# Kernel optimization log

Hardware: AMD Instinct MI355X
Metric: run time of the kernel (lower is better)

The kernel has to match this reference:

```python
import jax, jax.numpy as jnp
import numpy as np

N_NODES = 50000
N_EDGES = 600000
N_GRAPHS = 1000
IN_DIM = 16
HID = 128
DESC = 17
NUM_LAYERS = 3
BN_EPS = 1e-5


def setup_inputs() -> dict:
    key = jax.random.key(0)
    ks = jax.random.split(key, 16)
    x = jax.random.normal(ks[0], (N_NODES, IN_DIM), dtype=jnp.float32)
    edge_index = jax.random.randint(ks[1], (2, N_EDGES), 0, N_NODES, dtype=jnp.int32)
    edge_attr = jax.random.normal(ks[2], (N_EDGES, HID), dtype=jnp.float32)
    batch = jnp.sort(jax.random.randint(ks[3], (N_NODES,), 0, N_GRAPHS, dtype=jnp.int32))
    mol_desc = jax.random.normal(ks[4], (N_GRAPHS, DESC), dtype=jnp.float32)
    s = 1.0 / np.sqrt(HID)
    Wp = jax.random.normal(ks[5], (IN_DIM, HID), dtype=jnp.float32) / np.sqrt(IN_DIM)
    bp = jnp.zeros((HID,), jnp.float32)
    W1 = jax.random.normal(ks[6], (NUM_LAYERS, HID, HID), dtype=jnp.float32) * s
    b1 = jnp.zeros((NUM_LAYERS, HID), jnp.float32)
    W2 = jax.random.normal(ks[7], (NUM_LAYERS, HID, HID), dtype=jnp.float32) * s
    b2 = jnp.zeros((NUM_LAYERS, HID), jnp.float32)
    gamma = jnp.ones((NUM_LAYERS, HID), jnp.float32)
    beta = jnp.zeros((NUM_LAYERS, HID), jnp.float32)
    Wf = jax.random.normal(ks[8], (HID + DESC, 1), dtype=jnp.float32) / np.sqrt(HID + DESC)
    bf = jnp.zeros((1,), jnp.float32)
    return dict(x=x, edge_index=edge_index, edge_attr=edge_attr, batch=batch,
                mol_desc=mol_desc, Wp=Wp, bp=bp, W1=W1, b1=b1, W2=W2, b2=b2,
                gamma=gamma, beta=beta, Wf=Wf, bf=bf)


def reference(x, edge_index, edge_attr, batch, mol_desc,
              Wp, bp, W1, b1, W2, b2, gamma, beta, Wf, bf):
    src, dst = edge_index[0], edge_index[1]
    h = x @ Wp + bp  # [N, HID]
    for l in range(NUM_LAYERS):
        # GINEConv: aggr_i = sum_j relu(h_j + e_ij); out = MLP((1+eps)*h + aggr), eps=0
        msg = jax.nn.relu(h[src] + edge_attr)                       # [E, HID] gather
        aggr = jax.ops.segment_sum(msg, dst, num_segments=N_NODES)  # scatter-add
        z = h + aggr
        z = jax.nn.relu(z @ W1[l] + b1[l]) @ W2[l] + b2[l]
        # BatchNorm1d (training-mode batch statistics)
        mean = jnp.mean(z, axis=0)
        var = jnp.var(z, axis=0)
        z = (z - mean) * jax.lax.rsqrt(var + BN_EPS) * gamma[l] + beta[l]
        h = jax.nn.relu(z)  # dropout = identity (eval)
    # global mean pool per graph
    sums = jax.ops.segment_sum(h, batch, num_segments=N_GRAPHS)
    counts = jax.ops.segment_sum(jnp.ones((N_NODES,), h.dtype), batch, num_segments=N_GRAPHS)
    pooled = sums / jnp.maximum(counts, 1.0)[:, None]
    feats = jnp.concatenate([pooled, mol_desc], axis=1)  # [G, HID+DESC]
    return (feats @ Wf + bf).squeeze(-1)  # [G]
```

## Files before the change

kernel.cpp:

```cpp
#include <hip/hip_runtime.h>
#include <hip/hip_bf16.h>

#define NN 50000
#define NE 600000
#define NG 1000
#define IND 16
#define HID 128
#define DESCD 17
#define NL 3
#define BN_EPS 1e-5f
#define NB_SCAN 196

typedef short s16x8 __attribute__((ext_vector_type(8)));
typedef float f32x4 __attribute__((ext_vector_type(4)));
typedef float f32x2 __attribute__((ext_vector_type(2)));
typedef __hip_bfloat16 bfp16;
typedef __hip_bfloat162 bfp162;

__global__ __launch_bounds__(256) void k_hist(const int* __restrict__ dst,
                                              int* __restrict__ deg) {
    int e = blockIdx.x * blockDim.x + threadIdx.x;
    if (e >= NE) return;
    atomicAdd(&deg[dst[e]], 1);
}

__global__ __launch_bounds__(256) void k_part(const int* __restrict__ deg,
                                              int* __restrict__ partials) {
    __shared__ int sh[256];
    int i = blockIdx.x * 256 + threadIdx.x;
    sh[threadIdx.x] = (i < NN) ? deg[i] : 0;
    __syncthreads();
    for (int o = 128; o > 0; o >>= 1) {
        if (threadIdx.x < o) sh[threadIdx.x] += sh[threadIdx.x + o];
        __syncthreads();
    }
    if (threadIdx.x == 0) partials[blockIdx.x] = sh[0];
}

__global__ __launch_bounds__(256) void k_scanpart(const int* __restrict__ partials,
                                                  int* __restrict__ poffs) {
    __shared__ int sh[256];
    int t = threadIdx.x;
    int v = (t < NB_SCAN) ? partials[t] : 0;
    sh[t] = v;
    __syncthreads();
    for (int o = 1; o < 256; o <<= 1) {
        int tmp = (t >= o) ? sh[t - o] : 0;
        __syncthreads();
        sh[t] += tmp;
        __syncthreads();
    }
    if (t < NB_SCAN) poffs[t] = sh[t] - v;
}

__global__ __launch_bounds__(256) void k_scatter(const int* __restrict__ deg,
                                                 const int* __restrict__ poffs,
                                                 int* __restrict__ rowptr,
                                                 int* __restrict__ cursor) {
    __shared__ int sh[256];
    int b = blockIdx.x, t = threadIdx.x;
    int i = b * 256 + t;
    int v = (i < NN) ? deg[i] : 0;
    sh[t] = v;
    __syncthreads();
    for (int o = 1; o < 256; o <<= 1) {
        int tmp = (t >= o) ? sh[t - o] : 0;
        __syncthreads();
        sh[t] += tmp;
        __syncthreads();
    }
    int excl = sh[t] - v + poffs[b];
    if (i < NN) {
        rowptr[i] = excl;
        cursor[i] = excl;
        if (i == NN - 1) rowptr[NN] = excl + v;
    }
}

__global__ __launch_bounds__(256) void k_fill(const int* __restrict__ src,
                                              const int* __restrict__ dst,
                                              int* __restrict__ cursor,
                                              int2* __restrict__ perm) {
    int e = blockIdx.x * blockDim.x + threadIdx.x;
    if (e >= NE) return;
    int pos = atomicAdd(&cursor[dst[e]], 1);
    perm[pos] = make_int2(e, src[e]);
}

__global__ __launch_bounds__(256) void k_wprep(const float* __restrict__ W1,
                                               const float* __restrict__ W2,
                                               bfp16* __restrict__ Wt) {
    int id = blockIdx.x * blockDim.x + threadIdx.x;
    if (id >= 6 * HID * HID) return;
    int m = id >> 14;
    int rem = id & 16383;
    int n = rem >> 7, k = rem & 127;
    const float* Wsrc = (m < 3) ? (W1 + (size_t)m * HID * HID)
                                : (W2 + (size_t)(m - 3) * HID * HID);
    Wt[id] = __float2bfloat16(Wsrc[k * HID + n]);
}

__global__ __launch_bounds__(256) void k_proj(const float* __restrict__ x,
                                              const float* __restrict__ Wp,
                                              const float* __restrict__ bp,
                                              bfp16* __restrict__ h) {
    int idx = blockIdx.x * blockDim.x + threadIdx.x;
    if (idx >= NN * HID) return;
    int row = idx >> 7, col = idx & 127;
    const float* xr = x + (size_t)row * IND;
    float acc = bp[col];
#pragma unroll
    for (int k = 0; k < IND; k++) acc += xr[k] * Wp[k * HID + col];
    h[idx] = __float2bfloat16(acc);
}

template <int MODE, bool BN>
__global__ __launch_bounds__(256) void k_aggr(const bfp16* __restrict__ hz,
                                              const float* __restrict__ ea,
                                              bfp162* __restrict__ eab2,
                                              const int2* __restrict__ perm,
                                              const int* __restrict__ rowptr,
                                              const float* __restrict__ stats,
                                              const float* __restrict__ gamma,
                                              const float* __restrict__ beta,
                                              bfp16* __restrict__ z) {
    int nid = (blockIdx.x * blockDim.x + threadIdx.x) >> 6;
    int lane = threadIdx.x & 63;
    if (nid >= NN) return;
    const int f = lane * 2;

    float sc0 = 0.f, sf0 = 0.f, sc1 = 0.f, sf1 = 0.f;
    if (BN) {
        const float invn = 1.f / NN;
        float m0 = stats[f] * invn;
        float v0 = stats[128 + f] * invn - m0 * m0;
        sc0 = rsqrtf(v0 + BN_EPS) * gamma[f];
        sf0 = beta[f] - m0 * sc0;
        float m1 = stats[f + 1] * invn;
        float v1 = stats[128 + f + 1] * invn - m1 * m1;
        sc1 = rsqrtf(v1 + BN_EPS) * gamma[f + 1];
        sf1 = beta[f + 1] - m1 * sc1;
    }

    int beg = rowptr[nid], end = rowptr[nid + 1];
    float ax = 0.f, ay = 0.f;
    int i = beg;
    for (; i + 3 < end; i += 4) {
#pragma unroll
        for (int u = 0; u < 4; u++) {
            int2 pr = perm[i + u];
            float2 a;
            if (MODE == 2) {
                a = __bfloat1622float2(eab2[(size_t)(i + u) * 64 + lane]);
            } else {
                f32x2 av = __builtin_nontemporal_load(
                        (const f32x2*)&ea[(size_t)pr.x * HID + f]);
                a = make_float2(av.x, av.y);
                eab2[(size_t)(i + u) * 64 + lane] = __float22bfloat162_rn(a);
            }
            float2 hv = __bfloat1622float2(*(const bfp162*)&hz[(size_t)pr.y * HID + f]);
            if (BN) {
                hv.x = fmaxf(hv.x * sc0 + sf0, 0.f);
                hv.y = fmaxf(hv.y * sc1 + sf1, 0.f);
            }
            ax += fmaxf(a.x + hv.x, 0.f);
            ay += fmaxf(a.y + hv.y, 0.f);
        }
    }
    for (; i < end; i++) {
        int2 pr = perm[i];
        float2 a;
        if (MODE == 2) {
            a = __bfloat1622float2(eab2[(size_t)i * 64 + lane]);
        } else {
            f32x2 av = __builtin_nontemporal_load(
                    (const f32x2*)&ea[(size_t)pr.x * HID + f]);
            a = make_float2(av.x, av.y);
            eab2[(size_t)i * 64 + lane] = __float22bfloat162_rn(a);
        }
        float2 hv = __bfloat1622float2(*(const bfp162*)&hz[(size_t)pr.y * HID + f]);
        if (BN) {
            hv.x = fmaxf(hv.x * sc0 + sf0, 0.f);
            hv.y = fmaxf(hv.y * sc1 + sf1, 0.f);
        }
        ax += fmaxf(a.x + hv.x, 0.f);
        ay += fmaxf(a.y + hv.y, 0.f);
    }
    float2 hn = __bfloat1622float2(*(const bfp162*)&hz[(size_t)nid * HID + f]);
    if (BN) {
        hn.x = fmaxf(hn.x * sc0 + sf0, 0.f);
        hn.y = fmaxf(hn.y * sc1 + sf1, 0.f);
    }
    *(bfp162*)&z[(size_t)nid * HID + f] =
        __float22bfloat162_rn(make_float2(ax + hn.x, ay + hn.y));
}

__global__ __launch_bounds__(256) void k_mlp(const bfp16* __restrict__ A,
                                             const bfp16* __restrict__ Wt1,
                                             const bfp16* __restrict__ Wt2,
                                             const float* __restrict__ b1,
                                             const float* __restrict__ b2,
                                             bfp16* __restrict__ z2,
                                             float* __restrict__ stats,
                                             int N) {
    __shared__ __align__(16) short sW1[128 * 128];
    __shared__ __align__(16) short sW2[128 * 128];
    __shared__ __align__(16) short sA[64 * 128];
    const int t = threadIdx.x;
    const int rowBase = blockIdx.x * 64;

    const short* W1g = (const short*)Wt1;
    const short* W2g = (const short*)Wt2;
    for (int g = t; g < 2048; g += 256) {
        int nrow = g >> 4, s = g & 15;
        int sw = nrow * 128 + ((s ^ (nrow & 7)) << 3);
        *(float4*)&sW1[sw] = *(const float4*)&W1g[g * 8];
        *(float4*)&sW2[sw] = *(const float4*)&W2g[g * 8];
    }
    const short* Ag = (const short*)A;
    for (int g = t; g < 1024; g += 256) {
        int r = g >> 4, s = g & 15;
        float4 v = make_float4(0.f, 0.f, 0.f, 0.f);
        if (rowBase + r < N) v = *(const float4*)&Ag[(size_t)(rowBase + r) * 128 + s * 8];
        *(float4*)&sA[r * 128 + ((s ^ (r & 7)) << 3)] = v;
    }
    __syncthreads();

    const int w = t >> 6, lane = t & 63;
    const int l15 = lane & 15, lhi = lane >> 4;
    const int arow = (w << 4) + l15;
    const int abase = arow * 128, asw = arow & 7;
    const int bsw = l15 & 7;

    f32x4 acc[8];
#pragma unroll
    for (int c = 0; c < 8; c++) acc[c] = (f32x4){0.f, 0.f, 0.f, 0.f};
#pragma unroll
    for (int kk = 0; kk < 4; kk++) {
        int kslot = kk * 4 + lhi;
        s16x8 af = *(const s16x8*)&sA[abase + ((kslot ^ asw) << 3)];
#pragma unroll
        for (int c = 0; c < 8; c++) {
            s16x8 bfr = *(const s16x8*)&sW1[(c * 16 + l15) * 128 + ((kslot ^ bsw) << 3)];
            acc[c] = __builtin_amdgcn_mfma_f32_16x16x32_bf16(af, bfr, acc[c], 0, 0, 0);
        }
    }
    __syncthreads();

    {
        const int rowb = (w << 4);
#pragma unroll
        for (int c = 0; c < 8; c++) {
            float bb = b1[c * 16 + l15];
            int col = c * 16 + l15;
#pragma unroll
            for (int r = 0; r < 4; r++) {
                int row = rowb + lhi * 4 + r;
                float v = fmaxf(acc[c][r] + bb, 0.f);
                bfp16 bv = __float2bfloat16(v);
                sA[row * 128 + ((((col >> 3)) ^ (row & 7)) << 3) + (col & 7)] =
                    *reinterpret_cast<short*>(&bv);
            }
        }
    }
    __syncthreads();

    f32x4 acc2[8];
#pragma unroll
    for (int c = 0; c < 8; c++) acc2[c] = (f32x4){0.f, 0.f, 0.f, 0.f};
#pragma unroll
    for (int kk = 0; kk < 4; kk++) {
        int kslot = kk * 4 + lhi;
        s16x8 af = *(const s16x8*)&sA[abase + ((kslot ^ asw) << 3)];
#pragma unroll
        for (int c = 0; c < 8; c++) {
            s16x8 bfr = *(const s16x8*)&sW2[(c * 16 + l15) * 128 + ((kslot ^ bsw) << 3)];
            acc2[c] = __builtin_amdgcn_mfma_f32_16x16x32_bf16(af, bfr, acc2[c], 0, 0, 0);
        }
    }

    const int rb = rowBase + (w << 4) + lhi * 4;
    float scol[8], qcol[8];
#pragma unroll
    for (int c = 0; c < 8; c++) {
        float bb = b2[c * 16 + l15];
        float s = 0.f, q = 0.f;
#pragma unroll
        for (int r = 0; r < 4; r++) {
            int row = rb + r;
            float v = acc2[c][r] + bb;
            if (row < N) {
                z2[(size_t)row * 128 + c * 16 + l15] = __float2bfloat16(v);
                s += v;
                q += v * v;
            }
        }
        scol[c] = s;
        qcol[c] = q;
    }
#pragma unroll
    for (int c = 0; c < 8; c++) {
        scol[c] += __shfl_xor(scol[c], 16);
        scol[c] += __shfl_xor(scol[c], 32);
        qcol[c] += __shfl_xor(qcol[c], 16);
        qcol[c] += __shfl_xor(qcol[c], 32);
    }
    __syncthreads();
    float* sStat = (float*)sA;
    if (lane < 16) {
#pragma unroll
        for (int c = 0; c < 8; c++) {
            sStat[w * 256 + c * 16 + lane] = scol[c];
            sStat[w * 256 + 128 + c * 16 + lane] = qcol[c];
        }
    }
    __syncthreads();
    if (t < 128) {
        float ss = sStat[t] + sStat[256 + t] + sStat[512 + t] + sStat[768 + t];
        float qq = sStat[128 + t] + sStat[384 + t] + sStat[640 + t] + sStat[896 + t];
        atomicAdd(&stats[t], ss);
        atomicAdd(&stats[128 + t], qq);
    }
}

__global__ __launch_bounds__(256) void k_finalpool(const bfp16* __restrict__ z2,
                                                   const float* __restrict__ stats,
                                                   const float* __restrict__ gamma,
                                                   const float* __restrict__ beta,
                                                   const int* __restrict__ batch,
                                                   const float* __restrict__ mol,
                                                   const float* __restrict__ Wf,
                                                   const float* __restrict__ bfp,
                                                   float* __restrict__ out) {
    int gid = (blockIdx.x * blockDim.x + threadIdx.x) >> 6;
    int lane = threadIdx.x & 63;
    if (gid >= NG) return;
    const int f = lane * 2;

    const float invn = 1.f / NN;
    float m0 = stats[f] * invn;
    float v0 = stats[128 + f] * invn - m0 * m0;
    float sc0 = rsqrtf(v0 + BN_EPS) * gamma[f];
    float sf0 = beta[f] - m0 * sc0;
    float m1 = stats[f + 1] * invn;
    float v1 = stats[128 + f + 1] * invn - m1 * m1;
    float sc1 = rsqrtf(v1 + BN_EPS) * gamma[f + 1];
    float sf1 = beta[f + 1] - m1 * sc1;

    int lo = 0, hi = NN;
    while (lo < hi) { int m = (lo + hi) >> 1; if (batch[m] < gid) lo = m + 1; else hi = m; }
    int lb = lo;
    hi = NN;
    while (lo < hi) { int m = (lo + hi) >> 1; if (batch[m] <= gid) lo = m + 1; else hi = m; }
    int cnt = lo - lb;

    float sx = 0.f, sy = 0.f;
    for (int n = lb; n < lo; n++) {
        float2 v = __bfloat1622float2(*(const bfp162*)&z2[(size_t)n * HID + f]);
        sx += fmaxf(v.x * sc0 + sf0, 0.f);
        sy += fmaxf(v.y * sc1 + sf1, 0.f);
    }
    float inv = 1.f / fmaxf((float)cnt, 1.f);
    float acc = sx * inv * Wf[f] + sy * inv * Wf[f + 1];
    if (lane < DESCD) acc += mol[(size_t)gid * DESCD + lane] * Wf[HID + lane];
#pragma unroll
    for (int o = 32; o > 0; o >>= 1) acc += __shfl_down(acc, o);
    if (lane == 0) out[gid] = acc + bfp[0];
}

extern "C" void kernel_launch(void* const* d_in, const int* in_sizes, int n_in,
                              void* d_out, int out_size, void* d_ws, size_t ws_size,
                              hipStream_t stream) {
    const float* x     = (const float*)d_in[0];
    const int*   ei    = (const int*)d_in[1];
    const float* ea    = (const float*)d_in[2];
    const int*   batch = (const int*)d_in[3];
    const float* mol   = (const float*)d_in[4];
    const float* Wp    = (const float*)d_in[5];
    const float* bp    = (const float*)d_in[6];
    const float* W1    = (const float*)d_in[7];
    const float* b1    = (const float*)d_in[8];
    const float* W2    = (const float*)d_in[9];
    const float* b2    = (const float*)d_in[10];
    const float* gamma = (const float*)d_in[11];
    const float* beta  = (const float*)d_in[12];
    const float* Wf    = (const float*)d_in[13];
    const float* bf_   = (const float*)d_in[14];
    float* out = (float*)d_out;

    char* p = (char*)d_ws;
    size_t off = 0;
    auto alloc = [&](size_t bytes) {
        char* q = p + off;
        off = (off + bytes + 255) & ~(size_t)255;
        return q;
    };
    bfp16* h      = (bfp16*)alloc((size_t)NN * HID * 2);
    bfp16* z      = (bfp16*)alloc((size_t)NN * HID * 2);
    bfp16* z2     = (bfp16*)alloc((size_t)NN * HID * 2);
    bfp16* Wt     = (bfp16*)alloc((size_t)6 * HID * HID * 2);
    int2*  perm   = (int2*)alloc((size_t)NE * 8);
    int*   rowptr = (int*)alloc((NN + 16) * 4);
    int*   cursor = (int*)alloc(NN * 4);
    int*   partials = (int*)alloc(NB_SCAN * 4);
    int*   poffs    = (int*)alloc(NB_SCAN * 4);
    size_t zoff = off;
    int*   deg    = (int*)alloc(NN * 4);
    float* stats3 = (float*)alloc(3 * 256 * 4);
    size_t zlen = off - zoff;
    bfp162* eab2 = (bfp162*)alloc((size_t)NE * HID * 2);

    const int* src = ei;
    const int* dst = ei + NE;

    (void)hipMemsetAsync(p + zoff, 0, zlen, stream);
    k_hist<<<(NE + 255) / 256, 256, 0, stream>>>(dst, deg);
    k_part<<<NB_SCAN, 256, 0, stream>>>(deg, partials);
    k_scanpart<<<1, 256, 0, stream>>>(partials, poffs);
    k_scatter<<<NB_SCAN, 256, 0, stream>>>(deg, poffs, rowptr, cursor);
    k_fill<<<(NE + 255) / 256, 256, 0, stream>>>(src, dst, cursor, perm);
    k_wprep<<<(6 * HID * HID + 255) / 256, 256, 0, stream>>>(W1, W2, Wt);
    k_proj<<<(NN * HID) / 256, 256, 0, stream>>>(x, Wp, bp, h);

    const int aggrGrid = (NN * 64) / 256;
    const int mlpGrid = (NN + 63) / 64;
    for (int l = 0; l < NL; l++) {
        if (l == 0)
            k_aggr<1, false><<<aggrGrid, 256, 0, stream>>>(
                h, ea, eab2, perm, rowptr, nullptr, nullptr, nullptr, z);
        else
            k_aggr<2, true><<<aggrGrid, 256, 0, stream>>>(
                z2, nullptr, eab2, perm, rowptr, stats3 + (l - 1) * 256,
                gamma + (l - 1) * HID, beta + (l - 1) * HID, z);
        k_mlp<<<mlpGrid, 256, 0, stream>>>(
            z, Wt + (size_t)l * HID * HID, Wt + (size_t)(3 + l) * HID * HID,
            b1 + l * HID, b2 + l * HID, z2, stats3 + l * 256, NN);
    }

    k_finalpool<<<(NG * 64) / 256, 256, 0, stream>>>(
        z2, stats3 + 2 * 256, gamma + 2 * HID, beta + 2 * HID,
        batch, mol, Wf, bf_, out);
}
```

Measured before the change: 431.8 us.

## Split wavefront into four edge slots with 16-byte vector loads in aggregation

The aggregation kernel now gives each 16-lane group its own edge, with every lane handling 8 features through 16-byte loads of edge attributes and neighbour rows. The four partial sums are combined with cross-lane shuffles, and only 16 lanes write the output row. The aim is more memory-level parallelism per wavefront and fewer, wider memory transactions on the gather-heavy loop. Separately, the projection and weight-prep kernels are merged into a single launch to save one kernel launch. The cost is 16 extra accumulator and BN registers per lane, extra shuffles, and idle lanes for nodes with few edges.

After: 431.6 us. About the same (-0.1%).

```diff
diff --git a/kernel.cpp b/kernel.cpp
--- a/kernel.cpp
+++ b/kernel.cpp
@@ -13,9 +13,13 @@
 
 typedef short s16x8 __attribute__((ext_vector_type(8)));
 typedef float f32x4 __attribute__((ext_vector_type(4)));
-typedef float f32x2 __attribute__((ext_vector_type(2)));
+typedef int   i32x4 __attribute__((ext_vector_type(4)));
 typedef __hip_bfloat16 bfp16;
 typedef __hip_bfloat162 bfp162;
+
+__device__ __forceinline__ float b2f(short s) {
+    return __uint_as_float(((unsigned int)(unsigned short)s) << 16);
+}
 
 __global__ __launch_bounds__(256) void k_hist(const int* __restrict__ dst,
                                               int* __restrict__ deg) {
@@ -87,37 +91,39 @@
     perm[pos] = make_int2(e, src[e]);
 }
 
-__global__ __launch_bounds__(256) void k_wprep(const float* __restrict__ W1,
-                                               const float* __restrict__ W2,
-                                               bfp16* __restrict__ Wt) {
-    int id = blockIdx.x * blockDim.x + threadIdx.x;
-    if (id >= 6 * HID * HID) return;
-    int m = id >> 14;
-    int rem = id & 16383;
-    int n = rem >> 7, k = rem & 127;
-    const float* Wsrc = (m < 3) ? (W1 + (size_t)m * HID * HID)
-                                : (W2 + (size_t)(m - 3) * HID * HID);
-    Wt[id] = __float2bfloat16(Wsrc[k * HID + n]);
-}
-
-__global__ __launch_bounds__(256) void k_proj(const float* __restrict__ x,
-                                              const float* __restrict__ Wp,
-                                              const float* __restrict__ bp,
-                                              bfp16* __restrict__ h) {
-    int idx = blockIdx.x * blockDim.x + threadIdx.x;
-    if (idx >= NN * HID) return;
-    int row = idx >> 7, col = idx & 127;
-    const float* xr = x + (size_t)row * IND;
-    float acc = bp[col];
-#pragma unroll
-    for (int k = 0; k < IND; k++) acc += xr[k] * Wp[k * HID + col];
-    h[idx] = __float2bfloat16(acc);
+__global__ __launch_bounds__(256) void k_projwprep(const float* __restrict__ x,
+                                                   const float* __restrict__ Wp,
+                                                   const float* __restrict__ bp,
+                                                   bfp16* __restrict__ h,
+                                                   const float* __restrict__ W1,
+                                                   const float* __restrict__ W2,
+                                                   bfp16* __restrict__ Wt,
+                                                   int projBlocks) {
+    if (blockIdx.x < (unsigned)projBlocks) {
+        int idx = blockIdx.x * blockDim.x + threadIdx.x;
+        if (idx >= NN * HID) return;
+        int row = idx >> 7, col = idx & 127;
+        const float* xr = x + (size_t)row * IND;
+        float acc = bp[col];
+#pragma unroll
+        for (int k = 0; k < IND; k++) acc += xr[k] * Wp[k * HID + col];
+        h[idx] = __float2bfloat16(acc);
+    } else {
+        int id = (blockIdx.x - projBlocks) * blockDim.x + threadIdx.x;
+        if (id >= 6 * HID * HID) return;
+        int m = id >> 14;
+        int rem = id & 16383;
+        int n = rem >> 7, k = rem & 127;
+        const float* Wsrc = (m < 3) ? (W1 + (size_t)m * HID * HID)
+                                    : (W2 + (size_t)(m - 3) * HID * HID);
+        Wt[id] = __float2bfloat16(Wsrc[k * HID + n]);
+    }
 }
 
 template <int MODE, bool BN>
 __global__ __launch_bounds__(256) void k_aggr(const bfp16* __restrict__ hz,
                                               const float* __restrict__ ea,
-                                              bfp162* __restrict__ eab2,
+                                              bfp16* __restrict__ eab,
                                               const int2* __restrict__ perm,
                                               const int* __restrict__ rowptr,
                                               const float* __restrict__ stats,
@@ -127,72 +133,95 @@
     int nid = (blockIdx.x * blockDim.x + threadIdx.x) >> 6;
     int lane = threadIdx.x & 63;
     if (nid >= NN) return;
-    const int f = lane * 2;
-
-    float sc0 = 0.f, sf0 = 0.f, sc1 = 0.f, sf1 = 0.f;
+    const int slot = lane >> 4;
+    const int c0 = (lane & 15) << 3;
+
+    float sc[8], sf[8];
     if (BN) {
         const float invn = 1.f / NN;
-        float m0 = stats[f] * invn;
-        float v0 = stats[128 + f] * invn - m0 * m0;
-        sc0 = rsqrtf(v0 + BN_EPS) * gamma[f];
-        sf0 = beta[f] - m0 * sc0;
-        float m1 = stats[f + 1] * invn;
-        float v1 = stats[128 + f + 1] * invn - m1 * m1;
-        sc1 = rsqrtf(v1 + BN_EPS) * gamma[f + 1];
-        sf1 = beta[f + 1] - m1 * sc1;
-    }
+#pragma unroll
+        for (int j = 0; j < 8; j++) {
+            int c = c0 + j;
+            float m = stats[c] * invn;
+            float v = stats[128 + c] * invn - m * m;
+            sc[j] = rsqrtf(v + BN_EPS) * gamma[c];
+            sf[j] = beta[c] - m * sc[j];
+        }
+    }
+
+    float acc[8];
+#pragma unroll
+    for (int j = 0; j < 8; j++) acc[j] = 0.f;
+
+    auto body = [&](int i) {
+        int2 pr = perm[i];
+        float a[8];
+        if (MODE == 1) {
+            f32x4 a0 = __builtin_nontemporal_load(
+                (const f32x4*)&ea[(size_t)pr.x * HID + c0]);
+            f32x4 a1 = __builtin_nontemporal_load(
+                (const f32x4*)&ea[(size_t)pr.x * HID + c0 + 4]);
+            a[0] = a0.x; a[1] = a0.y; a[2] = a0.z; a[3] = a0.w;
+            a[4] = a1.x; a[5] = a1.y; a[6] = a1.z; a[7] = a1.w;
+            bfp162 p0 = __float22bfloat162_rn(make_float2(a[0], a[1]));
+            bfp162 p1 = __float22bfloat162_rn(make_float2(a[2], a[3]));
+            bfp162 p2 = __float22bfloat162_rn(make_float2(a[4], a[5]));
+            bfp162 p3 = __float22bfloat162_rn(make_float2(a[6], a[7]));
+            i32x4 o;
+            o.x = *reinterpret_cast<int*>(&p0);
+            o.y = *reinterpret_cast<int*>(&p1);
+            o.z = *reinterpret_cast<int*>(&p2);
+            o.w = *reinterpret_cast<int*>(&p3);
+            *(i32x4*)&eab[(size_t)i * HID + c0] = o;
+        } else {
+            s16x8 av = *(const s16x8*)&eab[(size_t)i * HID + c0];
+#pragma unroll
+            for (int j = 0; j < 8; j++) a[j] = b2f(av[j]);
+        }
+        s16x8 hv = *(const s16x8*)&hz[(size_t)pr.y * HID + c0];
+#pragma unroll
+        for (int j = 0; j < 8; j++) {
+            float hf = b2f(hv[j]);
+            if (BN) hf = fmaxf(hf * sc[j] + sf[j], 0.f);
+            acc[j] += fmaxf(a[j] + hf, 0.f);
+        }
+    };
 
     int beg = rowptr[nid], end = rowptr[nid + 1];
-    float ax = 0.f, ay = 0.f;
-    int i = beg;
-    for (; i + 3 < end; i += 4) {
-#pragma unroll
-        for (int u = 0; u < 4; u++) {
-            int2 pr = perm[i + u];
-            float2 a;
-            if (MODE == 2) {
-                a = __bfloat1622float2(eab2[(size_t)(i + u) * 64 + lane]);
-            } else {
-                f32x2 av = __builtin_nontemporal_load(
-                        (const f32x2*)&ea[(size_t)pr.x * HID + f]);
-                a = make_float2(av.x, av.y);
-                eab2[(size_t)(i + u) * 64 + lane] = __float22bfloat162_rn(a);
+    int i = beg + slot;
+    for (; i + 4 < end; i += 8) {
+        body(i);
+        body(i + 4);
+    }
+    if (i < end) body(i);
+
+#pragma unroll
+    for (int j = 0; j < 8; j++) {
+        acc[j] += __shfl_xor(acc[j], 16);
+        acc[j] += __shfl_xor(acc[j], 32);
+    }
+
+    if (lane < 16) {
+        s16x8 hv = *(const s16x8*)&hz[(size_t)nid * HID + c0];
+        bfp162 pk[4];
+#pragma unroll
+        for (int j = 0; j < 4; j++) {
+            float h0 = b2f(hv[2 * j]);
+            float h1 = b2f(hv[2 * j + 1]);
+            if (BN) {
+                h0 = fmaxf(h0 * sc[2 * j] + sf[2 * j], 0.f);
+                h1 = fmaxf(h1 * sc[2 * j + 1] + sf[2 * j + 1], 0.f);
             }
-            float2 hv = __bfloat1622float2(*(const bfp162*)&hz[(size_t)pr.y * HID + f]);
-            if (BN) {
-                hv.x = fmaxf(hv.x * sc0 + sf0, 0.f);
-                hv.y = fmaxf(hv.y * sc1 + sf1, 0.f);
-            }
-            ax += fmaxf(a.x + hv.x, 0.f);
-            ay += fmaxf(a.y + hv.y, 0.f);
-        }
-    }
-    for (; i < end; i++) {
-        int2 pr = perm[i];
-        float2 a;
-        if (MODE == 2) {
-            a = __bfloat1622float2(eab2[(size_t)i * 64 + lane]);
-        } else {
-            f32x2 av = __builtin_nontemporal_load(
-                    (const f32x2*)&ea[(size_t)pr.x * HID + f]);
-            a = make_float2(av.x, av.y);
-            eab2[(size_t)i * 64 + lane] = __float22bfloat162_rn(a);
-        }
-        float2 hv = __bfloat1622float2(*(const bfp162*)&hz[(size_t)pr.y * HID + f]);
-        if (BN) {
-            hv.x = fmaxf(hv.x * sc0 + sf0, 0.f);
-            hv.y = fmaxf(hv.y * sc1 + sf1, 0.f);
-        }
-        ax += fmaxf(a.x + hv.x, 0.f);
-        ay += fmaxf(a.y + hv.y, 0.f);
-    }
-    float2 hn = __bfloat1622float2(*(const bfp162*)&hz[(size_t)nid * HID + f]);
-    if (BN) {
-        hn.x = fmaxf(hn.x * sc0 + sf0, 0.f);
-        hn.y = fmaxf(hn.y * sc1 + sf1, 0.f);
-    }
-    *(bfp162*)&z[(size_t)nid * HID + f] =
-        __float22bfloat162_rn(make_float2(ax + hn.x, ay + hn.y));
+            pk[j] = __float22bfloat162_rn(make_float2(acc[2 * j] + h0,
+                                                      acc[2 * j + 1] + h1));
+        }
+        i32x4 o;
+        o.x = *reinterpret_cast<int*>(&pk[0]);
+        o.y = *reinterpret_cast<int*>(&pk[1]);
+        o.z = *reinterpret_cast<int*>(&pk[2]);
+        o.w = *reinterpret_cast<int*>(&pk[3]);
+        *(i32x4*)&z[(size_t)nid * HID + c0] = o;
+    }
 }
 
 __global__ __launch_bounds__(256) void k_mlp(const bfp16* __restrict__ A,
@@ -408,7 +437,7 @@
     int*   deg    = (int*)alloc(NN * 4);
     float* stats3 = (float*)alloc(3 * 256 * 4);
     size_t zlen = off - zoff;
-    bfp162* eab2 = (bfp162*)alloc((size_t)NE * HID * 2);
+    bfp16* eab    = (bfp16*)alloc((size_t)NE * HID * 2);
 
     const int* src = ei;
     const int* dst = ei + NE;
@@ -419,18 +448,22 @@
     k_scanpart<<<1, 256, 0, stream>>>(partials, poffs);
     k_scatter<<<NB_SCAN, 256, 0, stream>>>(deg, poffs, rowptr, cursor);
     k_fill<<<(NE + 255) / 256, 256, 0, stream>>>(src, dst, cursor, perm);
-    k_wprep<<<(6 * HID * HID + 255) / 256, 256, 0, stream>>>(W1, W2, Wt);
-    k_proj<<<(NN * HID) / 256, 256, 0, stream>>>(x, Wp, bp, h);
+    {
+        const int projBlocks = (NN * HID) / 256;
+        const int wprepBlocks = (6 * HID * HID + 255) / 256;
+        k_projwprep<<<projBlocks + wprepBlocks, 256, 0, stream>>>(
+            x, Wp, bp, h, W1, W2, Wt, projBlocks);
+    }
 
     const int aggrGrid = (NN * 64) / 256;
     const int mlpGrid = (NN + 63) / 64;
     for (int l = 0; l < NL; l++) {
         if (l == 0)
             k_aggr<1, false><<<aggrGrid, 256, 0, stream>>>(
-                h, ea, eab2, perm, rowptr, nullptr, nullptr, nullptr, z);
+                h, ea, eab, perm, rowptr, nullptr, nullptr, nullptr, z);
         else
             k_aggr<2, true><<<aggrGrid, 256, 0, stream>>>(
-                z2, nullptr, eab2, perm, rowptr, stats3 + (l - 1) * 256,
+                z2, nullptr, eab, perm, rowptr, stats3 + (l - 1) * 256,
                 gamma + (l - 1) * HID, beta + (l - 1) * HID, z);
         k_mlp<<<mlpGrid, 256, 0, stream>>>(
             z, Wt + (size_t)l * HID * HID, Wt + (size_t)(3 + l) * HID * HID,
```
